# Optimization experiments

Measured on AMD Instinct MI355X. Metric: run time of the kernel, lower is better.

Reference implementation:

```python
import jax, jax.numpy as jnp
import numpy as np

# CSSA config (index=0): H=W=64, strip windows h_spa=64, w_spa=8, heads=4, C=64
B, HW, C, HEADS = 32, 64, 64, 4
HS, WS = 64, 8          # h_spa, w_spa
HD = C // HEADS          # head_dim = 16
WIN = HS * WS            # 512 tokens per window
SCALE = HD ** -0.5


def setup_inputs() -> dict:
    key = jax.random.key(0)
    k1, k2, k3 = jax.random.split(key, 3)
    qkv = jax.random.normal(k1, (3, B, HW * HW, C), dtype=jnp.float32)
    w_conv = jax.random.normal(k2, (C, 1, 3, 3), dtype=jnp.float32) * 0.1
    b_conv = jax.random.normal(k3, (C,), dtype=jnp.float32) * 0.1
    return {"qkv": qkv, "w_conv": w_conv, "b_conv": b_conv}


def _to_img(x):
    # [B, N, C] -> [B, C, H, W]
    return jnp.transpose(x.reshape(B, HW, HW, C), (0, 3, 1, 2))


def _img2window_heads(x):
    img = _to_img(x)
    img = img.reshape(B, C, HW // HS, HS, HW // WS, WS)
    win = jnp.transpose(img, (0, 2, 4, 3, 5, 1)).reshape(-1, WIN, C)
    return jnp.transpose(win.reshape(-1, WIN, HEADS, HD), (0, 2, 1, 3))


def _v_windows(x):
    # [B, N, C] -> [B*nWin, C, h_spa, w_spa] (image-layout windows for conv)
    img = _to_img(x)
    img = img.reshape(B, C, HW // HS, HS, HW // WS, WS)
    return jnp.transpose(img, (0, 2, 4, 1, 3, 5)).reshape(-1, C, HS, WS)


def reference(qkv, w_conv, b_conv):
    q, k, v = qkv[0], qkv[1], qkv[2]
    qh = _img2window_heads(q) * SCALE
    kh = _img2window_heads(k)
    vw = _v_windows(v)                           # [Bw, C, HS, WS]
    # depthwise 3x3 conv LePE
    lepe = jax.lax.conv_general_dilated(
        vw, w_conv, window_strides=(1, 1), padding=((1, 1), (1, 1)),
        feature_group_count=C,
        dimension_numbers=("NCHW", "OIHW", "NCHW")) + b_conv[None, :, None, None]
    Bw = vw.shape[0]
    lepe = jnp.transpose(lepe.reshape(Bw, HEADS, HD, WIN), (0, 1, 3, 2))
    vh = jnp.transpose(vw.reshape(Bw, HEADS, HD, WIN), (0, 1, 3, 2))
    attn = jax.nn.softmax(jnp.einsum("whqd,whkd->whqk", qh, kh), axis=-1)
    x = jnp.einsum("whqk,whkd->whqd", attn, vh) + lepe
    x = jnp.transpose(x, (0, 2, 1, 3)).reshape(Bw, WIN, C)
    # window2spa
    x = x.reshape(B, HW // HS, HW // WS, HS, WS, C)
    x = jnp.transpose(x, (0, 1, 3, 2, 4, 5)).reshape(B, HW * HW, C)
    return x
```

## Files before the change

### kernel.cpp

```cpp
#include <hip/hip_runtime.h>
#include <stdint.h>

#define KSTR2 20
#define VSTR  520

typedef __attribute__((ext_vector_type(4))) short          short4v;
typedef __attribute__((ext_vector_type(4))) float          f32x4;
typedef __attribute__((ext_vector_type(4))) unsigned short us4;
typedef __bf16 bf2_t __attribute__((ext_vector_type(2)));

__device__ __forceinline__ unsigned short f2bf(float f) {
    union { float f; unsigned int u; } x; x.f = f;
    return (unsigned short)((x.u + 0x8000u) >> 16);
}
__device__ __forceinline__ float bf2f(unsigned short u) {
    union { unsigned int i; float f; } x; x.i = ((unsigned int)u) << 16; return x.f;
}
__device__ __forceinline__ unsigned int pk2bf(float lo, float hi) {
#if __has_builtin(__builtin_amdgcn_cvt_pk_bf16_f32)
    union { bf2_t v; unsigned int u; } c;
    c.v = __builtin_amdgcn_cvt_pk_bf16_f32(lo, hi);
    return c.u;
#else
    union { float f; unsigned int u; } a, b; a.f = lo; b.f = hi;
    return __builtin_amdgcn_perm(b.u + 0x8000u, a.u + 0x8000u, 0x07060302u);
#endif
}
__device__ __forceinline__ short4v pk4bf(float a, float b, float c, float d) {
    union { short4v s; unsigned int u[2]; } p;
    p.u[0] = pk2bf(a, b);
    p.u[1] = pk2bf(c, d);
    return p.s;
}

__global__ __launch_bounds__(512, 6)
void CSSA_69355131896243_kernel(const float* __restrict__ qkv,
                                const float* __restrict__ wconv,
                                const float* __restrict__ bconv,
                                float* __restrict__ out)
{
    __shared__ unsigned short Kl[512 * KSTR2];
    __shared__ unsigned short Vt[16 * VSTR];
    __shared__ float Wl[144];
    __shared__ float Bl[16];

    const int tid  = threadIdx.x;
    const int wave = tid >> 6, lane = tid & 63, quad = lane >> 4, l15 = lane & 15;

    const int bid = blockIdx.x;
    const int win = (bid & 7) * 32 + (bid >> 5);
    const int h   = (bid >> 3) & 3;
    const int b   = win >> 3, wx = win & 7;

    const size_t ONE  = (size_t)32 * 4096 * 64;
    const size_t base = ((size_t)b * 4096 + (size_t)wx * 8) * 64;
    const float* gQ = qkv + base;
    const float* gK = qkv + ONE + base;
    const float* gV = qkv + 2 * ONE + base;
    const int hc = h * 16;

    {
        const int c4 = tid & 3;
        const int t0 = tid >> 2;
        #pragma unroll
        for (int r = 0; r < 4; ++r) {
            const int t = r * 128 + t0;
            const size_t goff = (size_t)(t >> 3) * 4096 + (size_t)(t & 7) * 64 + hc + c4 * 4;
            f32x4 kd = *(const f32x4*)(gK + goff);
            f32x4 vd = *(const f32x4*)(gV + goff);
            us4 kb;
            #pragma unroll
            for (int j = 0; j < 4; ++j) kb[j] = f2bf(kd[j]);
            *(us4*)(&Kl[t * KSTR2 + c4 * 4]) = kb;
            #pragma unroll
            for (int j = 0; j < 4; ++j) Vt[(c4 * 4 + j) * VSTR + t] = f2bf(vd[j]);
        }
    }
    if (tid < 144) Wl[tid] = wconv[h * 144 + tid];
    if (tid < 16)  Bl[tid] = bconv[hc + tid];

    const float SCL = 0.25f * 1.44269504088896341f;
    const int q0 = wave * 64;
    short4v qf[4];
    #pragma unroll
    for (int t = 0; t < 4; ++t) {
        const int q = q0 + t * 16 + l15;
        f32x4 qv = *(const f32x4*)(gQ + (size_t)(q >> 3) * 4096 + (size_t)(q & 7) * 64 + hc + quad * 4);
        qf[t] = pk4bf(qv[0] * SCL, qv[1] * SCL, qv[2] * SCL, qv[3] * SCL);
    }
    __syncthreads();

    f32x4 acc[4];
    float lp[4];
    #pragma unroll
    for (int t = 0; t < 4; ++t) { acc[t] = (f32x4)0.0f; lp[t] = 0.0f; }

    #pragma unroll 4
    for (int c = 0; c < 32; ++c) {
        const short4v kf = *(const short4v*)(&Kl[(c * 16 + l15) * KSTR2 + quad * 4]);
        const short4v vf = *(const short4v*)(&Vt[l15 * VSTR + c * 16 + quad * 4]);
        #pragma unroll
        for (int t = 0; t < 4; ++t) {
            f32x4 s = __builtin_amdgcn_mfma_f32_16x16x16bf16_1k(kf, qf[t], (f32x4)0.0f, 0, 0, 0);
            const float p0 = __builtin_amdgcn_exp2f(s[0]);
            const float p1 = __builtin_amdgcn_exp2f(s[1]);
            const float p2 = __builtin_amdgcn_exp2f(s[2]);
            const float p3 = __builtin_amdgcn_exp2f(s[3]);
            lp[t] += (p0 + p1) + (p2 + p3);
            acc[t] = __builtin_amdgcn_mfma_f32_16x16x16bf16_1k(vf, pk4bf(p0, p1, p2, p3), acc[t], 0, 0, 0);
        }
    }

    float linv[4];
    #pragma unroll
    for (int t = 0; t < 4; ++t) {
        float v = lp[t];
        v += __shfl_xor(v, 16, 64);
        v += __shfl_xor(v, 32, 64);
        linv[t] = __builtin_amdgcn_rcpf(v);
    }

    #pragma unroll
    for (int j = 0; j < 4; ++j) {
        const int d = quad * 4 + j;
        float w9[9];
        #pragma unroll
        for (int o = 0; o < 9; ++o) w9[o] = Wl[d * 9 + o];
        const float bs = Bl[d];
        #pragma unroll
        for (int t = 0; t < 4; ++t) {
            const int q = q0 + t * 16 + l15;
            const int y = q >> 3, x = q & 7;
            float lep = bs;
            #pragma unroll
            for (int dy = 0; dy < 3; ++dy) {
                #pragma unroll
                for (int dx = 0; dx < 3; ++dx) {
                    const int yy = y + dy - 1, xx = x + dx - 1;
                    const bool ok = ((unsigned)yy < 64u) && ((unsigned)xx < 8u);
                    const int tt = (q + (dy - 1) * 8 + (dx - 1)) & 511;
                    lep += (ok ? w9[dy * 3 + dx] : 0.0f) * bf2f(Vt[d * VSTR + tt]);
                }
            }
            acc[t][j] = acc[t][j] * linv[t] + lep;
        }
    }
    float* gO = out + base;
    #pragma unroll
    for (int t = 0; t < 4; ++t) {
        const int q = q0 + t * 16 + l15;
        *(f32x4*)(gO + (size_t)(q >> 3) * 4096 + (size_t)(q & 7) * 64 + hc + quad * 4) = acc[t];
    }
}

extern "C" void kernel_launch(void* const* d_in, const int* in_sizes, int n_in,
                              void* d_out, int out_size, void* d_ws, size_t ws_size,
                              hipStream_t stream) {
    const float* qkv   = (const float*)d_in[0];
    const float* wconv = (const float*)d_in[1];
    const float* bconv = (const float*)d_in[2];
    float* outp = (float*)d_out;
    hipLaunchKernelGGL(CSSA_69355131896243_kernel, dim3(1024), dim3(512), 0, stream,
                       qkv, wconv, bconv, outp);
}
```

Measured before the change: 201.6 us.

## Split queries across two blocks and swizzle K/V shared-memory layouts

Doubles the grid so each block handles half of a window's 512 queries for one head, with 32 queries per wave instead of 64. K and V are restaged into fragment-ordered, XOR-swizzled shared-memory layouts so MFMA operand loads are contiguous and avoid bank conflicts, and V is stored without the strided transpose writes. Conversion to bf16 now uses packed conversion. The aim is more parallelism and cheaper LDS traffic, at the cost of each K/V tile being loaded and converted twice from global memory.

```diff
diff --git a/kernel.cpp b/kernel.cpp
--- a/kernel.cpp
+++ b/kernel.cpp
@@ -1,18 +1,12 @@
 #include <hip/hip_runtime.h>
 #include <stdint.h>
 
-#define KSTR2 20
-#define VSTR  520
 
 typedef __attribute__((ext_vector_type(4))) short          short4v;
 typedef __attribute__((ext_vector_type(4))) float          f32x4;
 typedef __attribute__((ext_vector_type(4))) unsigned short us4;
 typedef __bf16 bf2_t __attribute__((ext_vector_type(2)));
 
-__device__ __forceinline__ unsigned short f2bf(float f) {
-    union { float f; unsigned int u; } x; x.f = f;
-    return (unsigned short)((x.u + 0x8000u) >> 16);
-}
 __device__ __forceinline__ float bf2f(unsigned short u) {
     union { unsigned int i; float f; } x; x.i = ((unsigned int)u) << 16; return x.f;
 }
@@ -39,25 +33,26 @@
                                 const float* __restrict__ bconv,
                                 float* __restrict__ out)
 {
-    __shared__ unsigned short Kl[512 * KSTR2];
-    __shared__ unsigned short Vt[16 * VSTR];
+    __shared__ unsigned short Kl[8192];
+    __shared__ unsigned short Vl[8192];
     __shared__ float Wl[144];
     __shared__ float Bl[16];
 
     const int tid  = threadIdx.x;
     const int wave = tid >> 6, lane = tid & 63, quad = lane >> 4, l15 = lane & 15;
 
-    const int bid = blockIdx.x;
-    const int win = (bid & 7) * 32 + (bid >> 5);
-    const int h   = (bid >> 3) & 3;
-    const int b   = win >> 3, wx = win & 7;
+    const int bid  = blockIdx.x;
+    const int x    = bid & 7, s = (bid >> 3) & 7, y = bid >> 6;
+    const int head = s & 3, qh = s >> 2;
+    const int win  = x * 32 + y;
+    const int b    = win >> 3, wx = win & 7;
+    const int hc   = head * 16;
 
     const size_t ONE  = (size_t)32 * 4096 * 64;
     const size_t base = ((size_t)b * 4096 + (size_t)wx * 8) * 64;
     const float* gQ = qkv + base;
     const float* gK = qkv + ONE + base;
     const float* gV = qkv + 2 * ONE + base;
-    const int hc = h * 16;
 
     {
         const int c4 = tid & 3;
@@ -67,53 +62,65 @@
             const int t = r * 128 + t0;
             const size_t goff = (size_t)(t >> 3) * 4096 + (size_t)(t & 7) * 64 + hc + c4 * 4;
             f32x4 kd = *(const f32x4*)(gK + goff);
-            f32x4 vd = *(const f32x4*)(gV + goff);
-            us4 kb;
-            #pragma unroll
-            for (int j = 0; j < 4; ++j) kb[j] = f2bf(kd[j]);
-            *(us4*)(&Kl[t * KSTR2 + c4 * 4]) = kb;
-            #pragma unroll
-            for (int j = 0; j < 4; ++j) Vt[(c4 * 4 + j) * VSTR + t] = f2bf(vd[j]);
+            union { us4 v; unsigned int u[2]; } kb;
+            kb.u[0] = pk2bf(kd[0], kd[1]);
+            kb.u[1] = pk2bf(kd[2], kd[3]);
+            const int kidx = (t >> 4) * 256 + c4 * 64 + ((t & 15) ^ (c4 << 2)) * 4;
+            *(us4*)(&Kl[kidx]) = kb.v;
+        }
+        const int d = tid & 15;
+        #pragma unroll
+        for (int r = 0; r < 4; ++r) {
+            const int g = (tid >> 4) + r * 32;
+            const float* src = gV + (size_t)(g >> 1) * 4096 + (size_t)((g & 1) * 4) * 64 + hc + d;
+            const float v0 = src[0], v1 = src[64], v2 = src[128], v3 = src[192];
+            union { us4 v; unsigned int u[2]; } vb;
+            vb.u[0] = pk2bf(v0, v1);
+            vb.u[1] = pk2bf(v2, v3);
+            const int vidx = (g >> 2) * 256 + (g & 3) * 64 + d * 4;
+            *(us4*)(&Vl[vidx]) = vb.v;
         }
     }
-    if (tid < 144) Wl[tid] = wconv[h * 144 + tid];
+    if (tid < 144) Wl[tid] = wconv[head * 144 + tid];
     if (tid < 16)  Bl[tid] = bconv[hc + tid];
 
     const float SCL = 0.25f * 1.44269504088896341f;
-    const int q0 = wave * 64;
-    short4v qf[4];
+    const int q0 = qh * 256 + wave * 32;
+    short4v qf[2];
     #pragma unroll
-    for (int t = 0; t < 4; ++t) {
+    for (int t = 0; t < 2; ++t) {
         const int q = q0 + t * 16 + l15;
         f32x4 qv = *(const f32x4*)(gQ + (size_t)(q >> 3) * 4096 + (size_t)(q & 7) * 64 + hc + quad * 4);
         qf[t] = pk4bf(qv[0] * SCL, qv[1] * SCL, qv[2] * SCL, qv[3] * SCL);
     }
     __syncthreads();
 
-    f32x4 acc[4];
-    float lp[4];
+    f32x4 acc[2];
+    float lp[2];
     #pragma unroll
-    for (int t = 0; t < 4; ++t) { acc[t] = (f32x4)0.0f; lp[t] = 0.0f; }
+    for (int t = 0; t < 2; ++t) { acc[t] = (f32x4)0.0f; lp[t] = 0.0f; }
 
+    const int koff = quad * 64 + (l15 ^ (quad << 2)) * 4;
+    const int voff = quad * 64 + l15 * 4;
     #pragma unroll 4
     for (int c = 0; c < 32; ++c) {
-        const short4v kf = *(const short4v*)(&Kl[(c * 16 + l15) * KSTR2 + quad * 4]);
-        const short4v vf = *(const short4v*)(&Vt[l15 * VSTR + c * 16 + quad * 4]);
+        const short4v kf = *(const short4v*)(&Kl[koff + c * 256]);
+        const short4v vf = *(const short4v*)(&Vl[voff + c * 256]);
         #pragma unroll
-        for (int t = 0; t < 4; ++t) {
-            f32x4 s = __builtin_amdgcn_mfma_f32_16x16x16bf16_1k(kf, qf[t], (f32x4)0.0f, 0, 0, 0);
-            const float p0 = __builtin_amdgcn_exp2f(s[0]);
-            const float p1 = __builtin_amdgcn_exp2f(s[1]);
-            const float p2 = __builtin_amdgcn_exp2f(s[2]);
-            const float p3 = __builtin_amdgcn_exp2f(s[3]);
+        for (int t = 0; t < 2; ++t) {
+            f32x4 sc = __builtin_amdgcn_mfma_f32_16x16x16bf16_1k(kf, qf[t], (f32x4)0.0f, 0, 0, 0);
+            const float p0 = __builtin_amdgcn_exp2f(sc[0]);
+            const float p1 = __builtin_amdgcn_exp2f(sc[1]);
+            const float p2 = __builtin_amdgcn_exp2f(sc[2]);
+            const float p3 = __builtin_amdgcn_exp2f(sc[3]);
             lp[t] += (p0 + p1) + (p2 + p3);
             acc[t] = __builtin_amdgcn_mfma_f32_16x16x16bf16_1k(vf, pk4bf(p0, p1, p2, p3), acc[t], 0, 0, 0);
         }
     }
 
-    float linv[4];
+    float linv[2];
     #pragma unroll
-    for (int t = 0; t < 4; ++t) {
+    for (int t = 0; t < 2; ++t) {
         float v = lp[t];
         v += __shfl_xor(v, 16, 64);
         v += __shfl_xor(v, 32, 64);
@@ -122,24 +129,25 @@
 
     #pragma unroll
     for (int j = 0; j < 4; ++j) {
-        const int d = quad * 4 + j;
+        const int dbase = quad * 16 + j * 4;
         float w9[9];
         #pragma unroll
-        for (int o = 0; o < 9; ++o) w9[o] = Wl[d * 9 + o];
-        const float bs = Bl[d];
+        for (int o = 0; o < 9; ++o) w9[o] = Wl[(quad * 4 + j) * 9 + o];
+        const float bs = Bl[quad * 4 + j];
         #pragma unroll
-        for (int t = 0; t < 4; ++t) {
+        for (int t = 0; t < 2; ++t) {
             const int q = q0 + t * 16 + l15;
-            const int y = q >> 3, x = q & 7;
+            const int yy0 = q >> 3, xx0 = l15 & 7;
             float lep = bs;
             #pragma unroll
             for (int dy = 0; dy < 3; ++dy) {
                 #pragma unroll
                 for (int dx = 0; dx < 3; ++dx) {
-                    const int yy = y + dy - 1, xx = x + dx - 1;
+                    const int yy = yy0 + dy - 1, xx = xx0 + dx - 1;
                     const bool ok = ((unsigned)yy < 64u) && ((unsigned)xx < 8u);
                     const int tt = (q + (dy - 1) * 8 + (dx - 1)) & 511;
-                    lep += (ok ? w9[dy * 3 + dx] : 0.0f) * bf2f(Vt[d * VSTR + tt]);
+                    const int vi = (tt >> 4) * 256 + ((tt >> 2) & 3) * 64 + dbase + (tt & 3);
+                    lep += (ok ? w9[dy * 3 + dx] : 0.0f) * bf2f(Vl[vi]);
                 }
             }
             acc[t][j] = acc[t][j] * linv[t] + lep;
@@ -147,7 +155,7 @@
     }
     float* gO = out + base;
     #pragma unroll
-    for (int t = 0; t < 4; ++t) {
+    for (int t = 0; t < 2; ++t) {
         const int q = q0 + t * 16 + l15;
         *(f32x4*)(gO + (size_t)(q >> 3) * 4096 + (size_t)(q & 7) * 64 + hc + quad * 4) = acc[t];
     }
@@ -160,6 +168,6 @@
     const float* wconv = (const float*)d_in[1];
     const float* bconv = (const float*)d_in[2];
     float* outp = (float*)d_out;
-    hipLaunchKernelGGL(CSSA_69355131896243_kernel, dim3(1024), dim3(512), 0, stream,
+    hipLaunchKernelGGL(CSSA_69355131896243_kernel, dim3(2048), dim3(512), 0, stream,
                        qkv, wconv, bconv, outp);
 }
```

New measurement: 183.2 us. 9.1% less time.
